# Optimization experiments

Hardware: AMD Instinct MI355X
Metric: run time of the kernel (lower is better)

Reference implementation:

```python
import jax, jax.numpy as jnp
import numpy as np

P = 81        # provinces (sequence length)
E = 256       # H_ENC_COLS, encoder feature width per province
H = 4096      # stand-in for ORDER_VOCABULARY_SIZE (LSTMCell units)


def setup_inputs() -> dict:
    key = jax.random.key(0)
    k0, k1, k2, k3 = jax.random.split(key, 4)
    h_enc = jax.random.normal(k0, (P, E), dtype=jnp.float32)
    h0 = jax.random.normal(k1, (H,), dtype=jnp.float32) * 0.1  # tf.random.normal stddev=0.1
    W = jax.random.normal(k2, (E + H, 4 * H), dtype=jnp.float32) * 0.02  # input kernel
    U = jax.random.normal(k3, (H, 4 * H), dtype=jnp.float32) * 0.02      # recurrent kernel
    b = jnp.zeros((4 * H,), dtype=jnp.float32)
    return {"h_enc": h_enc, "h0": h0, "W": W, "U": U, "b": b}


def reference(h_enc, h0, W, U, b):
    # Keras LSTMCell(units=H, activation=None): gate order i,f,c,o;
    # recurrent_activation=sigmoid, candidate/output activation = identity.
    Hd = h0.shape[0]

    def step(carry, x_t):
        h, c = carry
        x = jnp.concatenate([x_t, h])            # [E+H] concat(province, h_dec)
        z = x @ W + h @ U + b                    # [4H]
        i, f, g, o = jnp.split(z, 4)
        i = jax.nn.sigmoid(i)
        f = jax.nn.sigmoid(f)
        o = jax.nn.sigmoid(o)
        c_new = f * c + i * g                    # activation=None -> linear candidate
        h_new = o * c_new                        # activation=None -> linear output
        return (h_new, c_new), h                 # emit pre-update h (= valid_orders)

    c0 = jnp.zeros((Hd,), dtype=h0.dtype)
    (_, _), orders = jax.lax.scan(step, (h0, c0), h_enc)
    return orders  # [P, H]
```

## Files before the change

### kernel.cpp

```cpp
#include <hip/hip_runtime.h>
#include <hip/hip_fp16.h>
#include <cstddef>

#define Pn 81
#define En 256
#define Hn 4096
#define H4 16384
#define KSPLIT 64
#define KC (Hn / KSPLIT)
#define CG 8
#define TT 16

__global__ __launch_bounds__(256) void xproj_kernel(const float* __restrict__ henc,
                                                    const float* __restrict__ W,
                                                    const float* __restrict__ bias,
                                                    float* __restrict__ X) {
    int col = blockIdx.x * 256 + threadIdx.x;
    int t0  = blockIdx.y * TT;
    __shared__ float hs[TT][En];
    for (int r = threadIdx.x; r < TT * En; r += 256) {
        int tt = r >> 8;
        int e  = r & (En - 1);
        hs[tt][e] = (t0 + tt < Pn) ? henc[(size_t)(t0 + tt) * En + e] : 0.f;
    }
    __syncthreads();
    float acc[TT];
    float bc = bias[col];
#pragma unroll
    for (int tt = 0; tt < TT; ++tt) acc[tt] = bc;
    for (int e = 0; e < En; ++e) {
        float w = W[(size_t)e * H4 + col];
#pragma unroll
        for (int tt = 0; tt < TT; ++tt) acc[tt] += hs[tt][e] * w;
    }
    int nt = Pn - t0; if (nt > TT) nt = TT;
    for (int tt = 0; tt < nt; ++tt) X[(size_t)(t0 + tt) * H4 + col] = acc[tt];
}

__global__ __launch_bounds__(256) void init_kernel(const float* __restrict__ h0,
                                                   float* __restrict__ orders,
                                                   float* __restrict__ c0) {
    int i = blockIdx.x * 256 + threadIdx.x;
    orders[i] = h0[i];
    c0[i] = 0.f;
}

__global__ __launch_bounds__(512) void fuse_step0_kernel(const float* __restrict__ W,
                                                         const float* __restrict__ U,
                                                         const float* __restrict__ h0,
                                                         __half* __restrict__ Mh,
                                                         float* __restrict__ zcur) {
    const int cg  = blockIdx.x;
    const int kc  = blockIdx.y;
    const int tid = threadIdx.x;
    __shared__ float hs[KC];
    if (tid < KC) hs[tid] = h0[kc * KC + tid];
    __syncthreads();

    const int half = tid >> 8;
    const int t256 = tid & 255;
    const int c0   = cg * 2048 + t256 * 8;

    float acc[8];
#pragma unroll
    for (int p = 0; p < 8; ++p) acc[p] = 0.f;

#pragma unroll 4
    for (int k = 0; k < 32; ++k) {
        const int krow = kc * KC + half * 32 + k;
        const float4* Wp = (const float4*)(W + (size_t)(En + krow) * H4 + c0);
        const float4* Up = (const float4*)(U + (size_t)krow * H4 + c0);
        float4 w0 = Wp[0], w1 = Wp[1];
        float4 u0 = Up[0], u1 = Up[1];
        float m[8];
        m[0] = w0.x + u0.x; m[1] = w0.y + u0.y; m[2] = w0.z + u0.z; m[3] = w0.w + u0.w;
        m[4] = w1.x + u1.x; m[5] = w1.y + u1.y; m[6] = w1.z + u1.z; m[7] = w1.w + u1.w;
        alignas(16) __half hm[8];
#pragma unroll
        for (int p = 0; p < 8; ++p) hm[p] = __float2half(m[p]);
        *(uint4*)(Mh + (size_t)krow * H4 + c0) = *(const uint4*)hm;
        float hk = hs[half * 32 + k];
#pragma unroll
        for (int p = 0; p < 8; ++p) acc[p] += hk * m[p];
    }

    __shared__ float accbuf[256][8];
    if (half == 1) {
#pragma unroll
        for (int p = 0; p < 8; ++p) accbuf[t256][p] = acc[p];
    }
    __syncthreads();
    if (half == 0) {
#pragma unroll
        for (int p = 0; p < 8; ++p) acc[p] += accbuf[t256][p];
        float4* zp = (float4*)(zcur + (size_t)kc * H4 + (size_t)c0);
        zp[0] = make_float4(acc[0], acc[1], acc[2], acc[3]);
        zp[1] = make_float4(acc[4], acc[5], acc[6], acc[7]);
    }
}

__global__ __launch_bounds__(512) void step_kernel(const __half* __restrict__ M,
                                                   const float* __restrict__ X,
                                                   const float* __restrict__ zprev,
                                                   float* __restrict__ zcur,
                                                   const float* __restrict__ cprev,
                                                   float* __restrict__ ccur,
                                                   float* __restrict__ orders,
                                                   int t) {
    const int cg  = blockIdx.x;
    const int kc  = blockIdx.y;
    const int tid = threadIdx.x;
    __shared__ float hs[KC];

    {
        const int lane = tid & 63;
        const int g    = tid >> 6;
        const int j    = kc * KC + lane;
        float s0 = 0.f, s1 = 0.f, s2 = 0.f, s3 = 0.f;
        for (int ks = g; ks < KSPLIT; ks += 8) {
            const float* zp = zprev + (size_t)ks * H4;
            s0 += zp[j];
            s1 += zp[j + Hn];
            s2 += zp[j + 2 * Hn];
            s3 += zp[j + 3 * Hn];
        }
        __shared__ float red[4][8][64];
        red[0][g][lane] = s0;
        red[1][g][lane] = s1;
        red[2][g][lane] = s2;
        red[3][g][lane] = s3;
        __syncthreads();
        if (g == 0) {
            const float* Xt = X + (size_t)(t - 1) * H4;
            float zi = Xt[j], zf = Xt[j + Hn], zg = Xt[j + 2 * Hn], zo = Xt[j + 3 * Hn];
#pragma unroll
            for (int g2 = 0; g2 < 8; ++g2) {
                zi += red[0][g2][lane];
                zf += red[1][g2][lane];
                zg += red[2][g2][lane];
                zo += red[3][g2][lane];
            }
            float gi = 1.f / (1.f + __expf(-zi));
            float gf = 1.f / (1.f + __expf(-zf));
            float go = 1.f / (1.f + __expf(-zo));
            float cn = gf * cprev[j] + gi * zg;
            float hn = go * cn;
            orders[(size_t)t * Hn + j] = hn;
            ccur[j] = cn;
            hs[lane] = hn;
        }
    }
    __syncthreads();

    const int half = tid >> 8;
    const int t256 = tid & 255;
    const int col8 = cg * 256 + t256;
    const uint4* M8 = (const uint4*)M;
    const size_t rowstride = H4 / 8;
    size_t base = (size_t)(kc * KC + half * 32) * rowstride + col8;
    float acc[8];
#pragma unroll
    for (int p = 0; p < 8; ++p) acc[p] = 0.f;
#pragma unroll 8
    for (int k = 0; k < 32; ++k) {
        uint4 raw = M8[base + (size_t)k * rowstride];
        float hk = hs[half * 32 + k];
        const __half2* hp = (const __half2*)&raw;
#pragma unroll
        for (int p = 0; p < 4; ++p) {
            float2 f = __half22float2(hp[p]);
            acc[2 * p]     += hk * f.x;
            acc[2 * p + 1] += hk * f.y;
        }
    }
    __shared__ float accbuf[256][8];
    if (half == 1) {
#pragma unroll
        for (int p = 0; p < 8; ++p) accbuf[t256][p] = acc[p];
    }
    __syncthreads();
    if (half == 0) {
#pragma unroll
        for (int p = 0; p < 8; ++p) acc[p] += accbuf[t256][p];
        float4* zp = (float4*)(zcur + (size_t)kc * H4 + (size_t)col8 * 8);
        zp[0] = make_float4(acc[0], acc[1], acc[2], acc[3]);
        zp[1] = make_float4(acc[4], acc[5], acc[6], acc[7]);
    }
}

__global__ __launch_bounds__(256) void final_gate_kernel(const float* __restrict__ zprev,
                                                         const float* __restrict__ X,
                                                         const float* __restrict__ cprev,
                                                         float* __restrict__ orders) {
    const int lane = threadIdx.x & 63;
    const int g    = threadIdx.x >> 6;
    const int j    = blockIdx.x * 64 + lane;
    float s0 = 0.f, s1 = 0.f, s2 = 0.f, s3 = 0.f;
    for (int ks = g; ks < KSPLIT; ks += 4) {
        const float* zp = zprev + (size_t)ks * H4;
        s0 += zp[j];
        s1 += zp[j + Hn];
        s2 += zp[j + 2 * Hn];
        s3 += zp[j + 3 * Hn];
    }
    __shared__ float red[4][4][64];
    red[0][g][lane] = s0;
    red[1][g][lane] = s1;
    red[2][g][lane] = s2;
    red[3][g][lane] = s3;
    __syncthreads();
    if (g == 0) {
        const float* Xt = X + (size_t)(Pn - 2) * H4;
        float zi = Xt[j]          + red[0][0][lane] + red[0][1][lane] + red[0][2][lane] + red[0][3][lane];
        float zf = Xt[j + Hn]     + red[1][0][lane] + red[1][1][lane] + red[1][2][lane] + red[1][3][lane];
        float zg = Xt[j + 2 * Hn] + red[2][0][lane] + red[2][1][lane] + red[2][2][lane] + red[2][3][lane];
        float zo = Xt[j + 3 * Hn] + red[3][0][lane] + red[3][1][lane] + red[3][2][lane] + red[3][3][lane];
        float gi = 1.f / (1.f + __expf(-zi));
        float gf = 1.f / (1.f + __expf(-zf));
        float go = 1.f / (1.f + __expf(-zo));
        float cn = gf * cprev[j] + gi * zg;
        orders[(size_t)(Pn - 1) * Hn + j] = go * cn;
    }
}

__global__ __launch_bounds__(256) void fb_init_kernel(const float* __restrict__ h0,
                                                      float* __restrict__ h,
                                                      float* __restrict__ c) {
    int i = blockIdx.x * 256 + threadIdx.x;
    h[i] = h0[i];
    c[i] = 0.f;
}

__global__ __launch_bounds__(256) void matvec2_kernel(const float* __restrict__ Wh,
                                                      const float* __restrict__ U,
                                                      const float* __restrict__ h,
                                                      float* __restrict__ zpart) {
    int col4 = blockIdx.x * 256 + threadIdx.x;
    int k0   = blockIdx.y * KC;
    __shared__ float hs[KC];
    if (threadIdx.x < KC) hs[threadIdx.x] = h[k0 + threadIdx.x];
    __syncthreads();
    const float4* W4 = (const float4*)Wh;
    const float4* U4 = (const float4*)U;
    size_t base = (size_t)k0 * (H4 / 4) + col4;
    float4 acc; acc.x = acc.y = acc.z = acc.w = 0.f;
#pragma unroll 2
    for (int k = 0; k < KC; ++k) {
        size_t idx = base + (size_t)k * (H4 / 4);
        float4 w = W4[idx];
        float4 u = U4[idx];
        float hk = hs[k];
        acc.x += hk * (w.x + u.x); acc.y += hk * (w.y + u.y);
        acc.z += hk * (w.z + u.z); acc.w += hk * (w.w + u.w);
    }
    ((float4*)zpart)[(size_t)blockIdx.y * (H4 / 4) + col4] = acc;
}

__global__ __launch_bounds__(256) void gate_kernel(const float* __restrict__ zpart,
                                                   const float* __restrict__ X,
                                                   float* __restrict__ h,
                                                   float* __restrict__ c,
                                                   float* __restrict__ orders,
                                                   int t) {
    int lane = threadIdx.x & 63;
    int g    = threadIdx.x >> 6;
    int j    = blockIdx.x * 64 + lane;
    float s0 = 0.f, s1 = 0.f, s2 = 0.f, s3 = 0.f;
    for (int ks = g; ks < KSPLIT; ks += 4) {
        const float* zp = zpart + (size_t)ks * H4;
        s0 += zp[j];
        s1 += zp[j + Hn];
        s2 += zp[j + 2 * Hn];
        s3 += zp[j + 3 * Hn];
    }
    __shared__ float red[4][4][64];
    red[0][g][lane] = s0;
    red[1][g][lane] = s1;
    red[2][g][lane] = s2;
    red[3][g][lane] = s3;
    __syncthreads();
    if (g == 0) {
        const float* Xt = X + (size_t)t * H4;
        float zi = Xt[j]          + red[0][0][lane] + red[0][1][lane] + red[0][2][lane] + red[0][3][lane];
        float zf = Xt[j + Hn]     + red[1][0][lane] + red[1][1][lane] + red[1][2][lane] + red[1][3][lane];
        float zg = Xt[j + 2 * Hn] + red[2][0][lane] + red[2][1][lane] + red[2][2][lane] + red[2][3][lane];
        float zo = Xt[j + 3 * Hn] + red[3][0][lane] + red[3][1][lane] + red[3][2][lane] + red[3][3][lane];
        float gi = 1.f / (1.f + __expf(-zi));
        float gf = 1.f / (1.f + __expf(-zf));
        float go = 1.f / (1.f + __expf(-zo));
        float cn = gf * c[j] + gi * zg;
        float ho = h[j];
        float hn = go * cn;
        orders[(size_t)t * Hn + j] = ho;
        h[j] = hn;
        c[j] = cn;
    }
}

extern "C" void kernel_launch(void* const* d_in, const int* in_sizes, int n_in,
                              void* d_out, int out_size, void* d_ws, size_t ws_size,
                              hipStream_t stream) {
    const float* henc = (const float*)d_in[0];
    const float* h0   = (const float*)d_in[1];
    const float* W    = (const float*)d_in[2];
    const float* U    = (const float*)d_in[3];
    const float* bias = (const float*)d_in[4];
    float* out = (float*)d_out;

    const size_t needM = (size_t)Hn * H4 * sizeof(__half);
    const size_t needX = (size_t)Pn * H4 * sizeof(float);
    const size_t needZ = (size_t)KSPLIT * H4 * sizeof(float);
    const size_t needC = (size_t)Hn * sizeof(float);

    char* ws = (char*)d_ws;
    const bool fused = ws_size >= needM + needX + 2 * needZ + 2 * needC;

    if (fused) {
        __half* Mh = (__half*)ws;
        float*  X  = (float*)(ws + needM);
        float*  zp[2];
        zp[0] = (float*)(ws + needM + needX);
        zp[1] = (float*)(ws + needM + needX + needZ);
        float* cb[2];
        cb[0] = (float*)(ws + needM + needX + 2 * needZ);
        cb[1] = cb[0] + Hn;

        xproj_kernel<<<dim3(H4 / 256, (Pn + TT - 1) / TT), 256, 0, stream>>>(henc, W, bias, X);
        init_kernel<<<dim3(Hn / 256), 256, 0, stream>>>(h0, out, cb[0]);
        fuse_step0_kernel<<<dim3(CG, KSPLIT), 512, 0, stream>>>(W, U, h0, Mh, zp[0]);

        for (int t = 1; t < Pn - 1; ++t) {
            step_kernel<<<dim3(CG, KSPLIT), 512, 0, stream>>>(
                Mh, X, zp[(t + 1) & 1], zp[t & 1],
                cb[(t + 1) & 1], cb[t & 1], out, t);
        }
        final_gate_kernel<<<dim3(Hn / 64), 256, 0, stream>>>(zp[1], X, cb[1], out);
    } else {
        float* X     = (float*)ws;
        float* zpart = (float*)(ws + needX);
        float* h     = (float*)(ws + needX + needZ);
        float* c     = h + Hn;

        xproj_kernel<<<dim3(H4 / 256, (Pn + TT - 1) / TT), 256, 0, stream>>>(henc, W, bias, X);
        fb_init_kernel<<<dim3(Hn / 256), 256, 0, stream>>>(h0, h, c);
        for (int t = 0; t < Pn; ++t) {
            matvec2_kernel<<<dim3(H4 / 4 / 256, KSPLIT), 256, 0, stream>>>(
                W + (size_t)En * H4, U, h, zpart);
            gate_kernel<<<dim3(Hn / 64), 256, 0, stream>>>(zpart, X, h, c, out, t);
        }
    }
}
```

Before: 2.318 ms.

## Tile recurrent fp16 matrix per block and prefetch it before gate reduction

Stores the fused W+U fp16 matrix in a blocked layout so each (kc, cg) block reads one contiguous slice, with rows interleaved between the two thread halves. The step kernel starts loading its first eight rows into registers before the cross-split gate reduction, then refills that buffer as it goes, so the weight stream overlaps the reduction and its syncs. The shared accumulation buffer is padded to avoid bank conflicts. The cost is more live registers for the prefetch buffer, which may lower occupancy.

```diff
diff --git a/kernel.cpp b/kernel.cpp
--- a/kernel.cpp
+++ b/kernel.cpp
@@ -10,6 +10,10 @@
 #define KC (Hn / KSPLIT)
 #define CG 8
 #define TT 16
+
+__device__ __forceinline__ size_t mt_slice(int kc, int cg) {
+    return ((size_t)(kc * CG + cg)) * (KC * 256);
+}
 
 __global__ __launch_bounds__(256) void xproj_kernel(const float* __restrict__ henc,
                                                     const float* __restrict__ W,
@@ -48,7 +52,7 @@
 __global__ __launch_bounds__(512) void fuse_step0_kernel(const float* __restrict__ W,
                                                          const float* __restrict__ U,
                                                          const float* __restrict__ h0,
-                                                         __half* __restrict__ Mh,
+                                                         __half* __restrict__ Mt,
                                                          float* __restrict__ zcur) {
     const int cg  = blockIdx.x;
     const int kc  = blockIdx.y;
@@ -60,6 +64,8 @@
     const int half = tid >> 8;
     const int t256 = tid & 255;
     const int c0   = cg * 2048 + t256 * 8;
+    uint4* M8 = (uint4*)Mt;
+    const size_t slice = mt_slice(kc, cg);
 
     float acc[8];
 #pragma unroll
@@ -78,13 +84,13 @@
         alignas(16) __half hm[8];
 #pragma unroll
         for (int p = 0; p < 8; ++p) hm[p] = __float2half(m[p]);
-        *(uint4*)(Mh + (size_t)krow * H4 + c0) = *(const uint4*)hm;
+        M8[slice + (size_t)(half * 32 + k) * 256 + t256] = *(const uint4*)hm;
         float hk = hs[half * 32 + k];
 #pragma unroll
         for (int p = 0; p < 8; ++p) acc[p] += hk * m[p];
     }
 
-    __shared__ float accbuf[256][8];
+    __shared__ float accbuf[256][9];
     if (half == 1) {
 #pragma unroll
         for (int p = 0; p < 8; ++p) accbuf[t256][p] = acc[p];
@@ -99,7 +105,7 @@
     }
 }
 
-__global__ __launch_bounds__(512) void step_kernel(const __half* __restrict__ M,
+__global__ __launch_bounds__(512) void step_kernel(const __half* __restrict__ Mt,
                                                    const float* __restrict__ X,
                                                    const float* __restrict__ zprev,
                                                    float* __restrict__ zcur,
@@ -110,8 +116,16 @@
     const int cg  = blockIdx.x;
     const int kc  = blockIdx.y;
     const int tid = threadIdx.x;
+    const int half = tid >> 8;
+    const int t256 = tid & 255;
+    const uint4* M8 = (const uint4*)Mt;
+    const size_t slice = mt_slice(kc, cg);
+
+    uint4 buf[8];
+#pragma unroll
+    for (int p = 0; p < 8; ++p) buf[p] = M8[slice + (size_t)p * 512 + tid];
+
     __shared__ float hs[KC];
-
     {
         const int lane = tid & 63;
         const int g    = tid >> 6;
@@ -152,28 +166,28 @@
     }
     __syncthreads();
 
-    const int half = tid >> 8;
-    const int t256 = tid & 255;
-    const int col8 = cg * 256 + t256;
-    const uint4* M8 = (const uint4*)M;
-    const size_t rowstride = H4 / 8;
-    size_t base = (size_t)(kc * KC + half * 32) * rowstride + col8;
     float acc[8];
 #pragma unroll
     for (int p = 0; p < 8; ++p) acc[p] = 0.f;
-#pragma unroll 8
-    for (int k = 0; k < 32; ++k) {
-        uint4 raw = M8[base + (size_t)k * rowstride];
-        float hk = hs[half * 32 + k];
-        const __half2* hp = (const __half2*)&raw;
-#pragma unroll
-        for (int p = 0; p < 4; ++p) {
-            float2 f = __half22float2(hp[p]);
-            acc[2 * p]     += hk * f.x;
-            acc[2 * p + 1] += hk * f.y;
-        }
-    }
-    __shared__ float accbuf[256][8];
+#pragma unroll
+    for (int kb = 0; kb < 32; kb += 8) {
+#pragma unroll
+        for (int p = 0; p < 8; ++p) {
+            uint4 raw = buf[p];
+            int kn = kb + p + 8;
+            if (kn < 32) buf[p] = M8[slice + (size_t)kn * 512 + tid];
+            float hk = hs[2 * (kb + p) + half];
+            const __half2* hp = (const __half2*)&raw;
+#pragma unroll
+            for (int q = 0; q < 4; ++q) {
+                float2 f = __half22float2(hp[q]);
+                acc[2 * q]     += hk * f.x;
+                acc[2 * q + 1] += hk * f.y;
+            }
+        }
+    }
+
+    __shared__ float accbuf[256][9];
     if (half == 1) {
 #pragma unroll
         for (int p = 0; p < 8; ++p) accbuf[t256][p] = acc[p];
@@ -182,7 +196,7 @@
     if (half == 0) {
 #pragma unroll
         for (int p = 0; p < 8; ++p) acc[p] += accbuf[t256][p];
-        float4* zp = (float4*)(zcur + (size_t)kc * H4 + (size_t)col8 * 8);
+        float4* zp = (float4*)(zcur + (size_t)kc * H4 + (size_t)(cg * 256 + t256) * 8);
         zp[0] = make_float4(acc[0], acc[1], acc[2], acc[3]);
         zp[1] = make_float4(acc[4], acc[5], acc[6], acc[7]);
     }
@@ -316,7 +330,7 @@
     const bool fused = ws_size >= needM + needX + 2 * needZ + 2 * needC;
 
     if (fused) {
-        __half* Mh = (__half*)ws;
+        __half* Mt = (__half*)ws;
         float*  X  = (float*)(ws + needM);
         float*  zp[2];
         zp[0] = (float*)(ws + needM + needX);
@@ -327,11 +341,11 @@
 
         xproj_kernel<<<dim3(H4 / 256, (Pn + TT - 1) / TT), 256, 0, stream>>>(henc, W, bias, X);
         init_kernel<<<dim3(Hn / 256), 256, 0, stream>>>(h0, out, cb[0]);
-        fuse_step0_kernel<<<dim3(CG, KSPLIT), 512, 0, stream>>>(W, U, h0, Mh, zp[0]);
+        fuse_step0_kernel<<<dim3(CG, KSPLIT), 512, 0, stream>>>(W, U, h0, Mt, zp[0]);
 
         for (int t = 1; t < Pn - 1; ++t) {
             step_kernel<<<dim3(CG, KSPLIT), 512, 0, stream>>>(
-                Mh, X, zp[(t + 1) & 1], zp[t & 1],
+                Mt, X, zp[(t + 1) & 1], zp[t & 1],
                 cb[(t + 1) & 1], cb[t & 1], out, t);
         }
         final_gate_kernel<<<dim3(Hn / 64), 256, 0, stream>>>(zp[1], X, cb[1], out);
```

Measured after the change: 2.464 ms. +6.3%, slower.
